# Kernel optimization log

Measured on AMD Instinct MI355X. Metric: run time of the kernel, lower is better.

The kernel has to match this reference:

```python
import jax, jax.numpy as jnp
import numpy as np

B, T, D_IN, D_FEAT, D_LAT = 256, 512, 128, 256, 512

def setup_inputs() -> dict:
    key = jax.random.key(0)
    ks = jax.random.split(key, 6)
    s = lambda fan_in: 1.0 / np.sqrt(fan_in)
    return {
        "x": jax.random.normal(ks[0], (B, T, D_IN), dtype=jnp.float32),
        "W_enc": jax.random.normal(ks[1], (D_IN, D_FEAT), dtype=jnp.float32) * s(D_IN),
        "b_enc": jnp.zeros((D_FEAT,), dtype=jnp.float32),
        "W_x": jax.random.normal(ks[2], (D_FEAT, 4 * D_LAT), dtype=jnp.float32) * s(D_FEAT),
        "W_h": jax.random.normal(ks[3], (D_LAT, 4 * D_LAT), dtype=jnp.float32) * s(D_LAT),
        "b_lstm": jnp.zeros((4 * D_LAT,), dtype=jnp.float32),
        "W_dec": jax.random.normal(ks[4], (D_LAT, 1), dtype=jnp.float32) * s(D_LAT),
        "b_dec": jnp.zeros((1,), dtype=jnp.float32),
    }

def reference(x, W_enc, b_enc, W_x, W_h, b_lstm, W_dec, b_dec):
    # Dense encoder with tanh: [B,T,D_IN] -> [B,T,D_FEAT]
    enc = jnp.tanh(jnp.einsum("bti,if->btf", x, W_enc) + b_enc)
    d = W_h.shape[0]
    # Precompute input-to-gate projection for all steps (hoisted out of loop)
    xz = jnp.einsum("btf,fg->btg", enc, W_x) + b_lstm  # [B,T,4d]
    xz_t = jnp.swapaxes(xz, 0, 1)  # [T,B,4d] for scan

    def step(carry, xz_step):
        h, c = carry
        z = xz_step + h @ W_h  # [B,4d]
        i, f, g, o = jnp.split(z, 4, axis=-1)  # Keras gate order: i,f,c,o
        i = jax.nn.sigmoid(i)
        f = jax.nn.sigmoid(f)
        g = jnp.tanh(g)
        o = jax.nn.sigmoid(o)
        c_new = f * c + i * g
        h_new = o * jnp.tanh(c_new)
        return (h_new, c_new), None

    h0 = jnp.zeros((x.shape[0], d), dtype=x.dtype)
    c0 = jnp.zeros((x.shape[0], d), dtype=x.dtype)
    (h_last, _), _ = jax.lax.scan(step, (h0, c0), xz_t)
    # Decoder on last hidden state: [B,d] -> [B,1]
    return h_last @ W_dec + b_dec
```

## Files before the change

### kernel.cpp

```cpp
#include <hip/hip_runtime.h>

#define BATCH 256
#define TLEN  512
#define DIN   128
#define DFEAT 256
#define DLAT  512
#define G4    2048
#define KCAT  768

typedef __bf16 bf16x8 __attribute__((ext_vector_type(8)));
typedef float f32x4 __attribute__((ext_vector_type(4)));

#define WCAT_OFF   0u
#define WENC_OFF   3145728u
#define ENC_OFF    3211264u
#define H_OFF      70320128u
#define FLAG_OFF   70844416u

__device__ __forceinline__ float sigf(float x)  { return 1.0f / (1.0f + __expf(-x)); }
__device__ __forceinline__ float tanhfast(float x){ return 2.0f / (1.0f + __expf(-2.0f * x)) - 1.0f; }
__device__ __forceinline__ unsigned short bfb(float f) {
    __bf16 b = (__bf16)f;
    return __builtin_bit_cast(unsigned short, b);
}

__global__ __launch_bounds__(256) void wprep_kernel(const float* __restrict__ Wx,
                                                    const float* __restrict__ Wh,
                                                    const float* __restrict__ Wenc,
                                                    __bf16* __restrict__ wcat,
                                                    __bf16* __restrict__ wencf) {
    int cid = blockIdx.x * 256 + threadIdx.x;
    float v[8];
    __bf16* dst;
    if (cid < 196608) {
        int widx = cid / 12288;
        int r1 = cid % 12288;
        int nn = r1 / 1536;
        int r2 = r1 % 1536;
        int ks = r2 >> 6, l = r2 & 63;
        int col = (nn >> 1) * 512 + widx * 32 + (nn & 1) * 16 + (l & 15);
        int kc = ks * 32 + (l >> 4) * 8;
#pragma unroll
        for (int j = 0; j < 8; ++j) {
            int kk = kc + j;
            v[j] = (kk < DFEAT) ? Wx[kk * G4 + col] : Wh[(kk - DFEAT) * G4 + col];
        }
        dst = wcat + (size_t)cid * 8;
    } else {
        int c2 = cid - 196608;
        int ntg = c2 >> 8;
        int r = c2 & 255;
        int ks = r >> 6, l = r & 63;
        int col = ntg * 16 + (l & 15);
        int kc = ks * 32 + (l >> 4) * 8;
#pragma unroll
        for (int j = 0; j < 8; ++j) v[j] = Wenc[(kc + j) * DFEAT + col];
        dst = wencf + (size_t)c2 * 8;
    }
    bf16x8 o;
#pragma unroll
    for (int j = 0; j < 8; ++j) o[j] = (__bf16)v[j];
    *reinterpret_cast<bf16x8*>(dst) = o;
}

__global__ __launch_bounds__(256) void enc_kernel(const float* __restrict__ x,
                                                  const float* __restrict__ benc,
                                                  const __bf16* __restrict__ wencf,
                                                  __bf16* __restrict__ enc) {
    __shared__ uint4 afrag4[1024];
    __bf16* afrag = reinterpret_cast<__bf16*>(afrag4);
    int tid = threadIdx.x;
    int lane = tid & 63, w = tid >> 6;
    int rid0 = blockIdx.x * 64;
    int ntg0 = blockIdx.y * 4;

    bf16x8 wr[4][4];
#pragma unroll
    for (int n = 0; n < 4; ++n)
#pragma unroll
        for (int ks = 0; ks < 4; ++ks)
            wr[n][ks] = *reinterpret_cast<const bf16x8*>(
                wencf + (size_t)(((ntg0 + n) * 4 + ks) * 64 + lane) * 8);
    float bias[4];
#pragma unroll
    for (int n = 0; n < 4; ++n) bias[n] = benc[(ntg0 + n) * 16 + (lane & 15)];

#pragma unroll
    for (int i = 0; i < 4; ++i) {
        int c = tid + 256 * i;
        int row = c >> 4, k8 = c & 15;
        const float* src = x + (size_t)(rid0 + row) * DIN + k8 * 8;
        float4 f0 = *reinterpret_cast<const float4*>(src);
        float4 f1 = *reinterpret_cast<const float4*>(src + 4);
        bf16x8 o;
        o[0] = (__bf16)f0.x; o[1] = (__bf16)f0.y; o[2] = (__bf16)f0.z; o[3] = (__bf16)f0.w;
        o[4] = (__bf16)f1.x; o[5] = (__bf16)f1.y; o[6] = (__bf16)f1.z; o[7] = (__bf16)f1.w;
        int l = (k8 & 3) * 16 + (row & 15);
        int a16 = ((row >> 4) * 4 + (k8 >> 2)) * 64 + l;
        *reinterpret_cast<bf16x8*>(afrag + (size_t)a16 * 8) = o;
    }
    __syncthreads();

    int m = w;
    f32x4 acc[4];
#pragma unroll
    for (int n = 0; n < 4; ++n) acc[n] = (f32x4){bias[n], bias[n], bias[n], bias[n]};
#pragma unroll
    for (int ks = 0; ks < 4; ++ks) {
        bf16x8 a = *reinterpret_cast<const bf16x8*>(afrag + (size_t)((m * 4 + ks) * 64 + lane) * 8);
#pragma unroll
        for (int n = 0; n < 4; ++n)
            acc[n] = __builtin_amdgcn_mfma_f32_16x16x32_bf16(a, wr[n][ks], acc[n], 0, 0, 0);
    }
#pragma unroll
    for (int n = 0; n < 4; ++n) {
        int colg = (ntg0 + n) * 16 + (lane & 15);
#pragma unroll
        for (int q = 0; q < 4; ++q) {
            int rid = rid0 + m * 16 + (lane >> 4) * 4 + q;
            int bb = rid >> 9, tt = rid & 511;
            float th = tanhfast(acc[n][q]);
            enc[(size_t)(tt * BATCH + bb) * DFEAT + colg] = (__bf16)th;
        }
    }
}

__global__ __launch_bounds__(256, 1) void lstm_kernel(const __bf16* __restrict__ enc,
                                                      const __bf16* __restrict__ wcat,
                                                      const float* __restrict__ blstm,
                                                      __bf16* __restrict__ hbuf,
                                                      unsigned int* __restrict__ flags) {
    extern __shared__ char smem[];
    __bf16* afrag = reinterpret_cast<__bf16*>(smem);
    float* zbuf = reinterpret_cast<float*>(smem + 24576);

    int tid = threadIdx.x;
    int lane = tid & 63, np = tid >> 6;
    int grp = blockIdx.x & 15, widx = blockIdx.x >> 4;
    int b0 = grp * 16;
    unsigned int* myflag = &flags[(grp * 16 + widx) * 16];

    bf16x8 wreg[2][24];
#pragma unroll
    for (int nt2 = 0; nt2 < 2; ++nt2)
#pragma unroll
        for (int ks = 0; ks < 24; ++ks)
            wreg[nt2][ks] = *reinterpret_cast<const bf16x8*>(
                wcat + (size_t)((((widx * 8 + np * 2 + nt2) * 24) + ks) * 64 + lane) * 8);
    float bias[2];
#pragma unroll
    for (int nt2 = 0; nt2 < 2; ++nt2)
        bias[nt2] = blstm[np * 512 + widx * 32 + nt2 * 16 + (lane & 15)];

    int cell = 2 * tid;
    int crow = cell >> 5, ccol = cell & 31;
    float c0 = 0.f, c1 = 0.f;

#pragma unroll 1
    for (int t = 0; t < TLEN; ++t) {
#pragma unroll
        for (int i = 0; i < 2; ++i) {
            int c = tid + 256 * i;
            int ks = c >> 6, l = c & 63;
            int row = l & 15;
            int k = ks * 32 + (l >> 4) * 8;
            uint4 d = *reinterpret_cast<const uint4*>(
                enc + (size_t)(t * BATCH + b0 + row) * DFEAT + k);
            *reinterpret_cast<uint4*>(afrag + (size_t)c * 8) = d;
        }
        __syncthreads();

        f32x4 acc[2];
        acc[0] = (f32x4){bias[0], bias[0], bias[0], bias[0]};
        acc[1] = (f32x4){bias[1], bias[1], bias[1], bias[1]};
#pragma unroll
        for (int ks = 0; ks < 8; ++ks) {
            bf16x8 a = *reinterpret_cast<const bf16x8*>(
                afrag + (size_t)((ks * 64 + lane) * 8));
            acc[0] = __builtin_amdgcn_mfma_f32_16x16x32_bf16(a, wreg[0][ks], acc[0], 0, 0, 0);
            acc[1] = __builtin_amdgcn_mfma_f32_16x16x32_bf16(a, wreg[1][ks], acc[1], 0, 0, 0);
        }

        if (t > 0) {
            if (tid < 64) {
                const unsigned int* f = &flags[(grp * 16 + (lane & 15)) * 16];
                unsigned v;
                do {
                    v = __hip_atomic_load(f, __ATOMIC_RELAXED, __HIP_MEMORY_SCOPE_AGENT);
                } while (!__all((int)(v >= (unsigned)t)));
            }
            __syncthreads();

            {
                const __bf16* hsrc = hbuf + (size_t)(t & 1) * (BATCH * DLAT);
                const __bf16* src[4];
                int cdst[4];
#pragma unroll
                for (int ii = 0; ii < 4; ++ii) {
                    int c = tid + 256 * (ii + 2);
                    int ks = c >> 6, l = c & 63;
                    int row = l & 15;
                    int kh = ks * 32 + (l >> 4) * 8 - DFEAT;
                    src[ii] = hsrc + (size_t)(b0 + row) * DLAT + kh;
                    cdst[ii] = c;
                }
                uint4 d0, d1, d2, d3;
                asm volatile(
                    "global_load_dwordx4 %0, %4, off sc1\n\t"
                    "global_load_dwordx4 %1, %5, off sc1\n\t"
                    "global_load_dwordx4 %2, %6, off sc1\n\t"
                    "global_load_dwordx4 %3, %7, off sc1\n\t"
                    "s_waitcnt vmcnt(0)"
                    : "=&v"(d0), "=&v"(d1), "=&v"(d2), "=&v"(d3)
                    : "v"(src[0]), "v"(src[1]), "v"(src[2]), "v"(src[3])
                    : "memory");
                *reinterpret_cast<uint4*>(afrag + (size_t)cdst[0] * 8) = d0;
                *reinterpret_cast<uint4*>(afrag + (size_t)cdst[1] * 8) = d1;
                *reinterpret_cast<uint4*>(afrag + (size_t)cdst[2] * 8) = d2;
                *reinterpret_cast<uint4*>(afrag + (size_t)cdst[3] * 8) = d3;
            }
            __syncthreads();

#pragma unroll
            for (int ks = 8; ks < 24; ++ks) {
                bf16x8 a = *reinterpret_cast<const bf16x8*>(
                    afrag + (size_t)((ks * 64 + lane) * 8));
                acc[0] = __builtin_amdgcn_mfma_f32_16x16x32_bf16(a, wreg[0][ks], acc[0], 0, 0, 0);
                acc[1] = __builtin_amdgcn_mfma_f32_16x16x32_bf16(a, wreg[1][ks], acc[1], 0, 0, 0);
            }
        }

#pragma unroll
        for (int nt2 = 0; nt2 < 2; ++nt2) {
#pragma unroll
            for (int q = 0; q < 4; ++q) {
                int rr = (lane >> 4) * 4 + q;
                zbuf[np * 512 + rr * 32 + nt2 * 16 + (lane & 15)] = acc[nt2][q];
            }
        }
        __syncthreads();

        float2 zi = *reinterpret_cast<float2*>(&zbuf[0 * 512 + crow * 32 + ccol]);
        float2 zf = *reinterpret_cast<float2*>(&zbuf[1 * 512 + crow * 32 + ccol]);
        float2 zg = *reinterpret_cast<float2*>(&zbuf[2 * 512 + crow * 32 + ccol]);
        float2 zo = *reinterpret_cast<float2*>(&zbuf[3 * 512 + crow * 32 + ccol]);
        float i0 = sigf(zi.x), f0 = sigf(zf.x), g0 = tanhfast(zg.x), o0 = sigf(zo.x);
        c0 = f0 * c0 + i0 * g0;
        float h0 = o0 * tanhfast(c0);
        float i1 = sigf(zi.y), f1 = sigf(zf.y), g1 = tanhfast(zg.y), o1 = sigf(zo.y);
        c1 = f1 * c1 + i1 * g1;
        float h1 = o1 * tanhfast(c1);

        unsigned int hp = (unsigned int)bfb(h0) | ((unsigned int)bfb(h1) << 16);
        unsigned int* hdst = reinterpret_cast<unsigned int*>(
            hbuf + (size_t)((t + 1) & 1) * (BATCH * DLAT) +
            (size_t)(b0 + crow) * DLAT + widx * 32 + ccol);
        __hip_atomic_store(hdst, hp, __ATOMIC_RELAXED, __HIP_MEMORY_SCOPE_AGENT);

        __syncthreads();
        if (tid == 0)
            __hip_atomic_store(myflag, (unsigned int)(t + 1), __ATOMIC_RELAXED,
                               __HIP_MEMORY_SCOPE_AGENT);
    }
}

__global__ __launch_bounds__(64) void dec_kernel(const __bf16* __restrict__ hbuf,
                                                 const float* __restrict__ wdec,
                                                 const float* __restrict__ bdec,
                                                 float* __restrict__ out) {
    int b = blockIdx.x, lane = threadIdx.x;
    uint4 d = *reinterpret_cast<const uint4*>(hbuf + (size_t)b * DLAT + lane * 8);
    const __bf16* hv = reinterpret_cast<const __bf16*>(&d);
    float4 w0 = *reinterpret_cast<const float4*>(wdec + lane * 8);
    float4 w1 = *reinterpret_cast<const float4*>(wdec + lane * 8 + 4);
    float s = (float)hv[0] * w0.x + (float)hv[1] * w0.y + (float)hv[2] * w0.z +
              (float)hv[3] * w0.w + (float)hv[4] * w1.x + (float)hv[5] * w1.y +
              (float)hv[6] * w1.z + (float)hv[7] * w1.w;
#pragma unroll
    for (int off = 32; off; off >>= 1) s += __shfl_xor(s, off);
    if (lane == 0) out[b] = s + bdec[0];
}

extern "C" void kernel_launch(void* const* d_in, const int* in_sizes, int n_in,
                              void* d_out, int out_size, void* d_ws, size_t ws_size,
                              hipStream_t stream) {
    (void)in_sizes; (void)n_in; (void)out_size; (void)ws_size;
    const float* x     = (const float*)d_in[0];
    const float* Wenc  = (const float*)d_in[1];
    const float* benc  = (const float*)d_in[2];
    const float* Wx    = (const float*)d_in[3];
    const float* Wh    = (const float*)d_in[4];
    const float* blstm = (const float*)d_in[5];
    const float* Wdec  = (const float*)d_in[6];
    const float* bdec  = (const float*)d_in[7];

    char* ws = (char*)d_ws;
    __bf16* wcat  = (__bf16*)(ws + WCAT_OFF);
    __bf16* wencf = (__bf16*)(ws + WENC_OFF);
    __bf16* enc   = (__bf16*)(ws + ENC_OFF);
    __bf16* hbuf  = (__bf16*)(ws + H_OFF);
    unsigned int* flags = (unsigned int*)(ws + FLAG_OFF);

    (void)hipMemsetAsync(ws + FLAG_OFF, 0, 16384, stream);

    wprep_kernel<<<784, 256, 0, stream>>>(Wx, Wh, Wenc, wcat, wencf);
    enc_kernel<<<dim3(2048, 4), 256, 0, stream>>>(x, benc, wencf, enc);

    (void)hipFuncSetAttribute(reinterpret_cast<const void*>(lstm_kernel),
                              hipFuncAttributeMaxDynamicSharedMemorySize, 90112);
    lstm_kernel<<<256, 256, 90112, stream>>>(enc, wcat, blstm, hbuf, flags);

    dec_kernel<<<256, 64, 0, stream>>>(hbuf, Wdec, bdec, (float*)d_out);
}
```

Measured before the change: 1.455 ms.

## Use per-wave flags and async enc prefetch to shorten LSTM step sync

```diff
diff --git a/kernel.cpp b/kernel.cpp
--- a/kernel.cpp
+++ b/kernel.cpp
@@ -10,6 +10,9 @@
 
 typedef __bf16 bf16x8 __attribute__((ext_vector_type(8)));
 typedef float f32x4 __attribute__((ext_vector_type(4)));
+
+typedef __attribute__((address_space(1))) const unsigned int glb_u32;
+typedef __attribute__((address_space(3))) unsigned int lds_u32;
 
 #define WCAT_OFF   0u
 #define WENC_OFF   3145728u
@@ -134,11 +137,10 @@
     __bf16* afrag = reinterpret_cast<__bf16*>(smem);
     float* zbuf = reinterpret_cast<float*>(smem + 24576);
 
-    int tid = threadIdx.x;
-    int lane = tid & 63, np = tid >> 6;
-    int grp = blockIdx.x & 15, widx = blockIdx.x >> 4;
-    int b0 = grp * 16;
-    unsigned int* myflag = &flags[(grp * 16 + widx) * 16];
+    const int tid = threadIdx.x;
+    const int lane = tid & 63, np = tid >> 6;
+    const int grp = blockIdx.x & 15, widx = blockIdx.x >> 4;
+    const int b0 = grp * 16;
 
     bf16x8 wreg[2][24];
 #pragma unroll
@@ -147,120 +149,110 @@
         for (int ks = 0; ks < 24; ++ks)
             wreg[nt2][ks] = *reinterpret_cast<const bf16x8*>(
                 wcat + (size_t)((((widx * 8 + np * 2 + nt2) * 24) + ks) * 64 + lane) * 8);
-    float bias[2];
-#pragma unroll
-    for (int nt2 = 0; nt2 < 2; ++nt2)
-        bias[nt2] = blstm[np * 512 + widx * 32 + nt2 * 16 + (lane & 15)];
-
-    int cell = 2 * tid;
-    int crow = cell >> 5, ccol = cell & 31;
+    const float bias0 = blstm[np * 512 + widx * 32 + (lane & 15)];
+    const float bias1 = blstm[np * 512 + widx * 32 + 16 + (lane & 15)];
+
+    const int row = tid & 15;
+    const int kq = (tid >> 6) * 32 + ((tid >> 4) & 3) * 8;
+    const __bf16* encp = enc + (size_t)(b0 + row) * DFEAT + kq;
+    const __bf16* hpA = hbuf + (size_t)(b0 + row) * DLAT + kq;
+    const __bf16* hpB = hpA + (size_t)BATCH * DLAT;
+    __bf16* enc_lds = afrag + tid * 8;
+    __bf16* h_lds = afrag + (512 + tid) * 8;
+    const int cell = 2 * tid;
+    const int crow = cell >> 5, ccol = cell & 31;
+    unsigned* hdA = reinterpret_cast<unsigned*>(
+        hbuf + (size_t)(b0 + crow) * DLAT + widx * 32 + ccol);
+    unsigned* hdB = reinterpret_cast<unsigned*>(
+        hbuf + (size_t)BATCH * DLAT + (size_t)(b0 + crow) * DLAT + widx * 32 + ccol);
+    const unsigned* pollp = &flags[(grp * 16 + (lane >> 2)) * 16 + (lane & 3)];
+    unsigned* myflag = &flags[(grp * 16 + widx) * 16 + np];
+    const float* zg = zbuf + crow * 32 + ccol;
+    float* zst = zbuf + np * 512 + ((lane >> 4) * 4) * 32 + (lane & 15);
+    const __bf16* abase = afrag + lane * 8;
+
     float c0 = 0.f, c1 = 0.f;
+
+    __builtin_amdgcn_global_load_lds((glb_u32*)encp, (lds_u32*)enc_lds, 16, 0, 0);
+    __builtin_amdgcn_global_load_lds((glb_u32*)(encp + 128), (lds_u32*)(enc_lds + 2048), 16, 0, 0);
+    encp += (size_t)BATCH * DFEAT;
+    __syncthreads();
 
 #pragma unroll 1
     for (int t = 0; t < TLEN; ++t) {
-#pragma unroll
-        for (int i = 0; i < 2; ++i) {
-            int c = tid + 256 * i;
-            int ks = c >> 6, l = c & 63;
-            int row = l & 15;
-            int k = ks * 32 + (l >> 4) * 8;
-            uint4 d = *reinterpret_cast<const uint4*>(
-                enc + (size_t)(t * BATCH + b0 + row) * DFEAT + k);
-            *reinterpret_cast<uint4*>(afrag + (size_t)c * 8) = d;
+        f32x4 acc0 = (f32x4){bias0, bias0, bias0, bias0};
+        f32x4 acc1 = (f32x4){bias1, bias1, bias1, bias1};
+#pragma unroll
+        for (int ks = 0; ks < 8; ++ks) {
+            bf16x8 a = *reinterpret_cast<const bf16x8*>(abase + ks * 512);
+            acc0 = __builtin_amdgcn_mfma_f32_16x16x32_bf16(a, wreg[0][ks], acc0, 0, 0, 0);
+            acc1 = __builtin_amdgcn_mfma_f32_16x16x32_bf16(a, wreg[1][ks], acc1, 0, 0, 0);
+        }
+
+        if (t > 0) {
+            unsigned v;
+            do {
+                v = __hip_atomic_load(pollp, __ATOMIC_RELAXED, __HIP_MEMORY_SCOPE_AGENT);
+            } while (!__all((int)(v >= (unsigned)t)));
+
+            const __bf16* hp = (t & 1) ? hpB : hpA;
+            uint4 d0, d1, d2, d3;
+            asm volatile(
+                "global_load_dwordx4 %0, %4, off sc1\n\t"
+                "global_load_dwordx4 %1, %4, off offset:256 sc1\n\t"
+                "global_load_dwordx4 %2, %4, off offset:512 sc1\n\t"
+                "global_load_dwordx4 %3, %4, off offset:768 sc1\n\t"
+                "s_waitcnt vmcnt(0)"
+                : "=&v"(d0), "=&v"(d1), "=&v"(d2), "=&v"(d3)
+                : "v"(hp) : "memory");
+            *reinterpret_cast<uint4*>(h_lds) = d0;
+            *reinterpret_cast<uint4*>(h_lds + 2048) = d1;
+            *reinterpret_cast<uint4*>(h_lds + 4096) = d2;
+            *reinterpret_cast<uint4*>(h_lds + 6144) = d3;
+            __syncthreads();
+
+#pragma unroll
+            for (int ks = 8; ks < 24; ++ks) {
+                bf16x8 a = *reinterpret_cast<const bf16x8*>(abase + ks * 512);
+                acc0 = __builtin_amdgcn_mfma_f32_16x16x32_bf16(a, wreg[0][ks], acc0, 0, 0, 0);
+                acc1 = __builtin_amdgcn_mfma_f32_16x16x32_bf16(a, wreg[1][ks], acc1, 0, 0, 0);
+            }
+        }
+
+#pragma unroll
+        for (int q = 0; q < 4; ++q) {
+            zst[q * 32] = acc0[q];
+            zst[q * 32 + 16] = acc1[q];
         }
         __syncthreads();
 
-        f32x4 acc[2];
-        acc[0] = (f32x4){bias[0], bias[0], bias[0], bias[0]};
-        acc[1] = (f32x4){bias[1], bias[1], bias[1], bias[1]};
-#pragma unroll
-        for (int ks = 0; ks < 8; ++ks) {
-            bf16x8 a = *reinterpret_cast<const bf16x8*>(
-                afrag + (size_t)((ks * 64 + lane) * 8));
-            acc[0] = __builtin_amdgcn_mfma_f32_16x16x32_bf16(a, wreg[0][ks], acc[0], 0, 0, 0);
-            acc[1] = __builtin_amdgcn_mfma_f32_16x16x32_bf16(a, wreg[1][ks], acc[1], 0, 0, 0);
-        }
-
-        if (t > 0) {
-            if (tid < 64) {
-                const unsigned int* f = &flags[(grp * 16 + (lane & 15)) * 16];
-                unsigned v;
-                do {
-                    v = __hip_atomic_load(f, __ATOMIC_RELAXED, __HIP_MEMORY_SCOPE_AGENT);
-                } while (!__all((int)(v >= (unsigned)t)));
-            }
-            __syncthreads();
-
-            {
-                const __bf16* hsrc = hbuf + (size_t)(t & 1) * (BATCH * DLAT);
-                const __bf16* src[4];
-                int cdst[4];
-#pragma unroll
-                for (int ii = 0; ii < 4; ++ii) {
-                    int c = tid + 256 * (ii + 2);
-                    int ks = c >> 6, l = c & 63;
-                    int row = l & 15;
-                    int kh = ks * 32 + (l >> 4) * 8 - DFEAT;
-                    src[ii] = hsrc + (size_t)(b0 + row) * DLAT + kh;
-                    cdst[ii] = c;
-                }
-                uint4 d0, d1, d2, d3;
-                asm volatile(
-                    "global_load_dwordx4 %0, %4, off sc1\n\t"
-                    "global_load_dwordx4 %1, %5, off sc1\n\t"
-                    "global_load_dwordx4 %2, %6, off sc1\n\t"
-                    "global_load_dwordx4 %3, %7, off sc1\n\t"
-                    "s_waitcnt vmcnt(0)"
-                    : "=&v"(d0), "=&v"(d1), "=&v"(d2), "=&v"(d3)
-                    : "v"(src[0]), "v"(src[1]), "v"(src[2]), "v"(src[3])
-                    : "memory");
-                *reinterpret_cast<uint4*>(afrag + (size_t)cdst[0] * 8) = d0;
-                *reinterpret_cast<uint4*>(afrag + (size_t)cdst[1] * 8) = d1;
-                *reinterpret_cast<uint4*>(afrag + (size_t)cdst[2] * 8) = d2;
-                *reinterpret_cast<uint4*>(afrag + (size_t)cdst[3] * 8) = d3;
-            }
-            __syncthreads();
-
-#pragma unroll
-            for (int ks = 8; ks < 24; ++ks) {
-                bf16x8 a = *reinterpret_cast<const bf16x8*>(
-                    afrag + (size_t)((ks * 64 + lane) * 8));
-                acc[0] = __builtin_amdgcn_mfma_f32_16x16x32_bf16(a, wreg[0][ks], acc[0], 0, 0, 0);
-                acc[1] = __builtin_amdgcn_mfma_f32_16x16x32_bf16(a, wreg[1][ks], acc[1], 0, 0, 0);
-            }
-        }
-
-#pragma unroll
-        for (int nt2 = 0; nt2 < 2; ++nt2) {
-#pragma unroll
-            for (int q = 0; q < 4; ++q) {
-                int rr = (lane >> 4) * 4 + q;
-                zbuf[np * 512 + rr * 32 + nt2 * 16 + (lane & 15)] = acc[nt2][q];
-            }
-        }
-        __syncthreads();
-
-        float2 zi = *reinterpret_cast<float2*>(&zbuf[0 * 512 + crow * 32 + ccol]);
-        float2 zf = *reinterpret_cast<float2*>(&zbuf[1 * 512 + crow * 32 + ccol]);
-        float2 zg = *reinterpret_cast<float2*>(&zbuf[2 * 512 + crow * 32 + ccol]);
-        float2 zo = *reinterpret_cast<float2*>(&zbuf[3 * 512 + crow * 32 + ccol]);
-        float i0 = sigf(zi.x), f0 = sigf(zf.x), g0 = tanhfast(zg.x), o0 = sigf(zo.x);
+        float2 zi = *reinterpret_cast<const float2*>(zg);
+        float2 zf = *reinterpret_cast<const float2*>(zg + 512);
+        float2 zgt = *reinterpret_cast<const float2*>(zg + 1024);
+        float2 zo = *reinterpret_cast<const float2*>(zg + 1536);
+        float i0 = sigf(zi.x), f0 = sigf(zf.x), g0 = tanhfast(zgt.x), o0 = sigf(zo.x);
         c0 = f0 * c0 + i0 * g0;
         float h0 = o0 * tanhfast(c0);
-        float i1 = sigf(zi.y), f1 = sigf(zf.y), g1 = tanhfast(zg.y), o1 = sigf(zo.y);
+        float i1 = sigf(zi.y), f1 = sigf(zf.y), g1 = tanhfast(zgt.y), o1 = sigf(zo.y);
         c1 = f1 * c1 + i1 * g1;
         float h1 = o1 * tanhfast(c1);
 
-        unsigned int hp = (unsigned int)bfb(h0) | ((unsigned int)bfb(h1) << 16);
-        unsigned int* hdst = reinterpret_cast<unsigned int*>(
-            hbuf + (size_t)((t + 1) & 1) * (BATCH * DLAT) +
-            (size_t)(b0 + crow) * DLAT + widx * 32 + ccol);
-        __hip_atomic_store(hdst, hp, __ATOMIC_RELAXED, __HIP_MEMORY_SCOPE_AGENT);
-
+        unsigned hpk = (unsigned)bfb(h0) | ((unsigned)bfb(h1) << 16);
+        __hip_atomic_store(((t & 1) ? hdA : hdB), hpk, __ATOMIC_RELAXED,
+                           __HIP_MEMORY_SCOPE_AGENT);
+
+        asm volatile("s_waitcnt vmcnt(0)" ::: "memory");
+        if (lane == 0)
+            __hip_atomic_store(myflag, (unsigned)(t + 1), __ATOMIC_RELAXED,
+                               __HIP_MEMORY_SCOPE_AGENT);
+
+        if (t + 1 < TLEN) {
+            __builtin_amdgcn_global_load_lds((glb_u32*)encp, (lds_u32*)enc_lds, 16, 0, 0);
+            __builtin_amdgcn_global_load_lds((glb_u32*)(encp + 128),
+                                             (lds_u32*)(enc_lds + 2048), 16, 0, 0);
+            encp += (size_t)BATCH * DFEAT;
+        }
         __syncthreads();
-        if (tid == 0)
-            __hip_atomic_store(myflag, (unsigned int)(t + 1), __ATOMIC_RELAXED,
-                               __HIP_MEMORY_SCOPE_AGENT);
     }
 }
 
```

Measured after the change: 1.539 ms. +5.8%, slower.

## Interleave LSTM gate columns so gates combine in registers, dropping LDS z-buffer

Applied to the files above, without the earlier changes.

```diff
diff --git a/kernel.cpp b/kernel.cpp
--- a/kernel.cpp
+++ b/kernel.cpp
@@ -38,7 +38,10 @@
         int nn = r1 / 1536;
         int r2 = r1 % 1536;
         int ks = r2 >> 6, l = r2 & 63;
-        int col = (nn >> 1) * 512 + widx * 32 + (nn & 1) * 16 + (l & 15);
+        int np = nn >> 1, nf = nn & 1;
+        int cc = l & 15;
+        int gate = (cc < 8) ? (nf ? 2 : 0) : (nf ? 3 : 1);
+        int col = gate * 512 + widx * 32 + np * 8 + (cc & 7);
         int kc = ks * 32 + (l >> 4) * 8;
 #pragma unroll
         for (int j = 0; j < 8; ++j) {
@@ -132,7 +135,6 @@
                                                       unsigned int* __restrict__ flags) {
     extern __shared__ char smem[];
     __bf16* afrag = reinterpret_cast<__bf16*>(smem);
-    float* zbuf = reinterpret_cast<float*>(smem + 24576);
 
     int tid = threadIdx.x;
     int lane = tid & 63, np = tid >> 6;
@@ -142,19 +144,24 @@
 
     bf16x8 wreg[2][24];
 #pragma unroll
-    for (int nt2 = 0; nt2 < 2; ++nt2)
+    for (int nf = 0; nf < 2; ++nf)
 #pragma unroll
         for (int ks = 0; ks < 24; ++ks)
-            wreg[nt2][ks] = *reinterpret_cast<const bf16x8*>(
-                wcat + (size_t)((((widx * 8 + np * 2 + nt2) * 24) + ks) * 64 + lane) * 8);
-    float bias[2];
-#pragma unroll
-    for (int nt2 = 0; nt2 < 2; ++nt2)
-        bias[nt2] = blstm[np * 512 + widx * 32 + nt2 * 16 + (lane & 15)];
-
-    int cell = 2 * tid;
-    int crow = cell >> 5, ccol = cell & 31;
+            wreg[nf][ks] = *reinterpret_cast<const bf16x8*>(
+                wcat + (size_t)(((((widx * 4 + np) * 2 + nf) * 24) + ks) * 64 + lane) * 8);
+
+    const int cbase = widx * 32 + np * 8 + (lane & 7);
+    const bool lo = (lane & 15) < 8;
+    const float bias0 = blstm[(lo ? 0 : 1) * 512 + cbase];
+    const float bias1 = blstm[(lo ? 2 : 3) * 512 + cbase];
+
     float c0 = 0.f, c1 = 0.f;
+    const int srow = (lane >> 4) * 4 + (lo ? 0 : 2) + (lane & 1);
+    const int scol = widx * 32 + np * 8 + (lane & 6);
+    unsigned* hdA = reinterpret_cast<unsigned*>(
+        hbuf + (size_t)(b0 + srow) * DLAT + scol);
+    unsigned* hdB = reinterpret_cast<unsigned*>(
+        hbuf + (size_t)BATCH * DLAT + (size_t)(b0 + srow) * DLAT + scol);
 
 #pragma unroll 1
     for (int t = 0; t < TLEN; ++t) {
@@ -170,15 +177,14 @@
         }
         __syncthreads();
 
-        f32x4 acc[2];
-        acc[0] = (f32x4){bias[0], bias[0], bias[0], bias[0]};
-        acc[1] = (f32x4){bias[1], bias[1], bias[1], bias[1]};
+        f32x4 acc0 = (f32x4){bias0, bias0, bias0, bias0};
+        f32x4 acc1 = (f32x4){bias1, bias1, bias1, bias1};
 #pragma unroll
         for (int ks = 0; ks < 8; ++ks) {
             bf16x8 a = *reinterpret_cast<const bf16x8*>(
                 afrag + (size_t)((ks * 64 + lane) * 8));
-            acc[0] = __builtin_amdgcn_mfma_f32_16x16x32_bf16(a, wreg[0][ks], acc[0], 0, 0, 0);
-            acc[1] = __builtin_amdgcn_mfma_f32_16x16x32_bf16(a, wreg[1][ks], acc[1], 0, 0, 0);
+            acc0 = __builtin_amdgcn_mfma_f32_16x16x32_bf16(a, wreg[0][ks], acc0, 0, 0, 0);
+            acc1 = __builtin_amdgcn_mfma_f32_16x16x32_bf16(a, wreg[1][ks], acc1, 0, 0, 0);
         }
 
         if (t > 0) {
@@ -225,37 +231,34 @@
             for (int ks = 8; ks < 24; ++ks) {
                 bf16x8 a = *reinterpret_cast<const bf16x8*>(
                     afrag + (size_t)((ks * 64 + lane) * 8));
-                acc[0] = __builtin_amdgcn_mfma_f32_16x16x32_bf16(a, wreg[0][ks], acc[0], 0, 0, 0);
-                acc[1] = __builtin_amdgcn_mfma_f32_16x16x32_bf16(a, wreg[1][ks], acc[1], 0, 0, 0);
+                acc0 = __builtin_amdgcn_mfma_f32_16x16x32_bf16(a, wreg[0][ks], acc0, 0, 0, 0);
+                acc1 = __builtin_amdgcn_mfma_f32_16x16x32_bf16(a, wreg[1][ks], acc1, 0, 0, 0);
             }
         }
 
-#pragma unroll
-        for (int nt2 = 0; nt2 < 2; ++nt2) {
-#pragma unroll
-            for (int q = 0; q < 4; ++q) {
-                int rr = (lane >> 4) * 4 + q;
-                zbuf[np * 512 + rr * 32 + nt2 * 16 + (lane & 15)] = acc[nt2][q];
-            }
-        }
-        __syncthreads();
-
-        float2 zi = *reinterpret_cast<float2*>(&zbuf[0 * 512 + crow * 32 + ccol]);
-        float2 zf = *reinterpret_cast<float2*>(&zbuf[1 * 512 + crow * 32 + ccol]);
-        float2 zg = *reinterpret_cast<float2*>(&zbuf[2 * 512 + crow * 32 + ccol]);
-        float2 zo = *reinterpret_cast<float2*>(&zbuf[3 * 512 + crow * 32 + ccol]);
-        float i0 = sigf(zi.x), f0 = sigf(zf.x), g0 = tanhfast(zg.x), o0 = sigf(zo.x);
-        c0 = f0 * c0 + i0 * g0;
-        float h0 = o0 * tanhfast(c0);
-        float i1 = sigf(zi.y), f1 = sigf(zf.y), g1 = tanhfast(zg.y), o1 = sigf(zo.y);
-        c1 = f1 * c1 + i1 * g1;
-        float h1 = o1 * tanhfast(c1);
-
-        unsigned int hp = (unsigned int)bfb(h0) | ((unsigned int)bfb(h1) << 16);
-        unsigned int* hdst = reinterpret_cast<unsigned int*>(
-            hbuf + (size_t)((t + 1) & 1) * (BATCH * DLAT) +
-            (size_t)(b0 + crow) * DLAT + widx * 32 + ccol);
-        __hip_atomic_store(hdst, hp, __ATOMIC_RELAXED, __HIP_MEMORY_SCOPE_AGENT);
+        float p00 = __shfl_xor(acc0[0], 8), p01 = __shfl_xor(acc0[1], 8);
+        float p02 = __shfl_xor(acc0[2], 8), p03 = __shfl_xor(acc0[3], 8);
+        float p10 = __shfl_xor(acc1[0], 8), p11 = __shfl_xor(acc1[1], 8);
+        float p12 = __shfl_xor(acc1[2], 8), p13 = __shfl_xor(acc1[3], 8);
+
+        float zi_a = lo ? acc0[0] : p02, zf_a = lo ? p00 : acc0[2];
+        float zg_a = lo ? acc1[0] : p12, zo_a = lo ? p10 : acc1[2];
+        float zi_b = lo ? acc0[1] : p03, zf_b = lo ? p01 : acc0[3];
+        float zg_b = lo ? acc1[1] : p13, zo_b = lo ? p11 : acc1[3];
+
+        float ia = sigf(zi_a), fa = sigf(zf_a), ga = tanhfast(zg_a), oa = sigf(zo_a);
+        c0 = fa * c0 + ia * ga;
+        float h_a = oa * tanhfast(c0);
+        float ib = sigf(zi_b), fb = sigf(zf_b), gb = tanhfast(zg_b), ob = sigf(zo_b);
+        c1 = fb * c1 + ib * gb;
+        float h_b = ob * tanhfast(c1);
+
+        unsigned sendv = (lane & 1) ? (unsigned)bfb(h_a) : (unsigned)bfb(h_b);
+        unsigned recv = (unsigned)__shfl_xor((int)sendv, 1);
+        unsigned word = (lane & 1) ? (recv | ((unsigned)bfb(h_b) << 16))
+                                   : ((unsigned)bfb(h_a) | (recv << 16));
+        __hip_atomic_store(((t & 1) ? hdA : hdB), word, __ATOMIC_RELAXED,
+                           __HIP_MEMORY_SCOPE_AGENT);
 
         __syncthreads();
         if (tid == 0)
```

Result: slower. 1.501 ms (+3.2%).
